# Performance work log

Measured on AMD Instinct MI355X. Metric: run time of the kernel, lower is better.

Reference implementation:

```python
import jax, jax.numpy as jnp
import numpy as np

CUTOFF = 5.2
BOX = 44.0
N_ATOMS = 8192

# 13 half-shifts used by the cell list (vector_index_displacement) + zero shift
HALF_SHIFTS = np.array([
    [-1, 0, 0], [-1, -1, 0], [0, -1, 0], [1, -1, 0],
    [-1, 1, -1], [0, 1, -1], [1, 1, -1], [-1, 0, -1],
    [0, 0, -1], [1, 0, -1], [-1, -1, -1], [0, -1, -1], [1, -1, -1]], dtype=np.int64)
ALL_SHIFTS = np.concatenate([np.zeros((1, 3), dtype=np.int64), HALF_SHIFTS], axis=0)  # (14,3)


def setup_inputs() -> dict:
    key = jax.random.key(0)
    k1, k2 = jax.random.split(key)
    species = jax.random.randint(k1, (1, N_ATOMS), 0, 4, dtype=jnp.int64)
    coordinates = jax.random.uniform(k2, (1, N_ATOMS, 3), dtype=jnp.float32) * BOX
    cell = jnp.eye(3, dtype=jnp.float32) * BOX
    pbc = jnp.ones((3,), dtype=bool)
    return {"species": species, "coordinates": coordinates, "cell": cell, "pbc": pbc}


def reference(species, coordinates, cell, pbc):
    # Single molecule, as asserted by the torch module.
    coords = coordinates[0]  # (N, 3)
    n = coords.shape[0]
    # map_to_central: wrap coordinates into the central cell
    frac = coords @ jnp.linalg.inv(cell)
    frac = frac - jnp.floor(frac)
    coords = frac @ cell
    # orthorhombic cell diagonal (norm of cell columns, as in _setup_variables)
    diag = jnp.linalg.norm(cell, axis=0)  # (3,)

    shifts = jnp.asarray(ALL_SHIFTS)
    pairs_list, shift_list = [], []
    cutoff2 = CUTOFF * CUTOFF
    for k in range(shifts.shape[0]):  # fixed small loop over 14 periodic shifts
        s = shifts[k]
        # delta[i, j] = r_i - r_j + s * cell_diagonal   (N, N, 3)
        delta = coords[:, None, :] - coords[None, :, :] + s.astype(coords.dtype) * diag
        d2 = jnp.sum(delta * delta, axis=-1)  # (N, N)
        mask = d2 <= cutoff2
        if k == 0:
            # within-image pairs: each unordered pair once, no self pairs
            mask = jnp.triu(mask, 1)
        i, j = jnp.nonzero(mask)  # eager: data-dependent pair count
        pairs_list.append(jnp.stack([i, j], axis=0))
        shift_list.append(jnp.broadcast_to(s, (i.shape[0], 3)))
    atom_pairs = jnp.concatenate(pairs_list, axis=1)  # (2, P)
    shift_indices = jnp.concatenate(shift_list, axis=0)  # (P, 3)
    return atom_pairs, shift_indices


if __name__ == "__main__":
    out = reference(**setup_inputs())
    print(out[0].shape, out[1].shape)
```

## Files before the change

kernel.cpp:

```cpp
#include <hip/hip_runtime.h>

#define CLB_NATOMS 8192
#define CLB_NSHIFT 14
#define CLB_NROWS (CLB_NSHIFT * CLB_NATOMS)
#define CLB_NTILE 112
#define CLB_NCELL 512
#define CLB_CAP 128
#define CLB_C2 ((float)(5.2 * 5.2))
#define CLB_R 5.35f

__device__ const int clb_shifts[CLB_NSHIFT][3] = {
    {0, 0, 0},
    {-1, 0, 0}, {-1, -1, 0}, {0, -1, 0}, {1, -1, 0},
    {-1, 1, -1}, {0, 1, -1}, {1, 1, -1}, {-1, 0, -1},
    {0, 0, -1}, {1, 0, -1}, {-1, -1, -1}, {0, -1, -1}, {1, -1, -1}};

__device__ float4 clb_pp[CLB_NATOMS];
__device__ float4 clb_sorted[CLB_NATOMS];
__device__ unsigned clb_hist[CLB_NCELL];
__device__ unsigned clb_cstart[CLB_NCELL + 1];
__device__ unsigned clb_cfill[CLB_NCELL];
__device__ int clb_jbuf[(size_t)CLB_NROWS * CLB_CAP];
__device__ unsigned clb_cnt[CLB_NROWS];
__device__ unsigned clb_off[CLB_NROWS];
__device__ unsigned clb_tot[CLB_NTILE];
__device__ float4 clb_dg;
__device__ float4 clb_cinv;
__device__ float4 clb_sf[CLB_NSHIFT];

__global__ __launch_bounds__(512) void clb_setup(const float* __restrict__ cell) {
  int t = threadIdx.x;
  if (t < CLB_NCELL) clb_hist[t] = 0u;
  if (t == 0) {
    float dgx = (float)sqrt((double)cell[0] * cell[0] + (double)cell[3] * cell[3] +
                            (double)cell[6] * cell[6]);
    float dgy = (float)sqrt((double)cell[1] * cell[1] + (double)cell[4] * cell[4] +
                            (double)cell[7] * cell[7]);
    float dgz = (float)sqrt((double)cell[2] * cell[2] + (double)cell[5] * cell[5] +
                            (double)cell[8] * cell[8]);
    clb_dg = make_float4(dgx, dgy, dgz, 0.f);
    clb_cinv = make_float4(8.0f / dgx, 8.0f / dgy, 8.0f / dgz, 0.f);
    for (int k = 0; k < CLB_NSHIFT; ++k)
      clb_sf[k] = make_float4(__fmul_rn((float)clb_shifts[k][0], dgx),
                              __fmul_rn((float)clb_shifts[k][1], dgy),
                              __fmul_rn((float)clb_shifts[k][2], dgz), 0.f);
  }
}

__device__ __forceinline__ int clb_cellof(const float4& p, const float4& cinv) {
  int cx = min(7, (int)(p.x * cinv.x));
  int cy = min(7, (int)(p.y * cinv.y));
  int cz = min(7, (int)(p.z * cinv.z));
  return (cz * 8 + cy) * 8 + cx;
}

__global__ __launch_bounds__(256) void clb_wrapbin(const float* __restrict__ coords,
                                                   const float* __restrict__ cell) {
  int i = blockIdx.x * blockDim.x + threadIdx.x;
  if (i >= CLB_NATOMS) return;
  double a00 = cell[0], a01 = cell[1], a02 = cell[2];
  double a10 = cell[3], a11 = cell[4], a12 = cell[5];
  double a20 = cell[6], a21 = cell[7], a22 = cell[8];
  double det = a00 * (a11 * a22 - a12 * a21) - a01 * (a10 * a22 - a12 * a20) +
               a02 * (a10 * a21 - a11 * a20);
  double id = 1.0 / det;
  float inv[3][3];
  inv[0][0] = (float)((a11 * a22 - a12 * a21) * id);
  inv[0][1] = (float)(-(a01 * a22 - a02 * a21) * id);
  inv[0][2] = (float)((a01 * a12 - a02 * a11) * id);
  inv[1][0] = (float)(-(a10 * a22 - a12 * a20) * id);
  inv[1][1] = (float)((a00 * a22 - a02 * a20) * id);
  inv[1][2] = (float)(-(a00 * a12 - a02 * a10) * id);
  inv[2][0] = (float)((a10 * a21 - a11 * a20) * id);
  inv[2][1] = (float)(-(a00 * a21 - a01 * a20) * id);
  inv[2][2] = (float)((a00 * a11 - a01 * a10) * id);

  float x = coords[3 * i], y = coords[3 * i + 1], z = coords[3 * i + 2];
  float fr[3], w[3];
#pragma unroll
  for (int c = 0; c < 3; ++c) {
    float f = __fadd_rn(__fadd_rn(__fmul_rn(x, inv[0][c]), __fmul_rn(y, inv[1][c])),
                        __fmul_rn(z, inv[2][c]));
    fr[c] = __fsub_rn(f, floorf(f));
  }
#pragma unroll
  for (int c = 0; c < 3; ++c) {
    w[c] = __fadd_rn(
        __fadd_rn(__fmul_rn(fr[0], cell[0 * 3 + c]), __fmul_rn(fr[1], cell[1 * 3 + c])),
        __fmul_rn(fr[2], cell[2 * 3 + c]));
  }
  float4 p = make_float4(w[0], w[1], w[2], 0.0f);
  clb_pp[i] = p;
  atomicAdd(&clb_hist[clb_cellof(p, clb_cinv)], 1u);
}

__global__ __launch_bounds__(512) void clb_cscan() {
  __shared__ unsigned sd[512];
  int t = threadIdx.x;
  unsigned v = clb_hist[t];
  sd[t] = v;
  __syncthreads();
  unsigned acc = v;
  for (int off = 1; off < 512; off <<= 1) {
    unsigned a = (t >= off) ? sd[t - off] : 0u;
    __syncthreads();
    acc += a;
    sd[t] = acc;
    __syncthreads();
  }
  clb_cstart[t] = acc - v;
  clb_cfill[t] = acc - v;
  if (t == 511) clb_cstart[512] = acc;
}

__global__ __launch_bounds__(256) void clb_scatter() {
  int i = blockIdx.x * blockDim.x + threadIdx.x;
  if (i >= CLB_NATOMS) return;
  float4 p = clb_pp[i];
  int c = clb_cellof(p, clb_cinv);
  unsigned pos = atomicAdd(&clb_cfill[c], 1u);
  p.w = __int_as_float(i);
  clb_sorted[pos] = p;
}

__device__ __forceinline__ bool clb_alive(float xi, float yi, float zi, int sx, int sy,
                                          int sz, float dgx, float dgy, float dgz) {
  bool a = true;
  if (sx < 0) a = a && (xi >= dgx - 5.3f); else if (sx > 0) a = a && (xi <= 5.3f);
  if (sy < 0) a = a && (yi >= dgy - 5.3f); else if (sy > 0) a = a && (yi <= 5.3f);
  if (sz < 0) a = a && (zi >= dgz - 5.3f); else if (sz > 0) a = a && (zi <= 5.3f);
  return a;
}

__device__ __forceinline__ void clb_crange(float t, float ci, int& lo, int& hi) {
  lo = max(0, (int)(fmaxf(t - CLB_R, 0.f) * ci));
  hi = min(7, (int)(fmaxf(t + CLB_R, 0.f) * ci));
}

__device__ __forceinline__ unsigned clb_iscan(unsigned v, int lane) {
  for (int off = 1; off < 64; off <<= 1) {
    unsigned t = __shfl_up(v, off);
    if (lane >= off) v += t;
  }
  return v;
}

__global__ __launch_bounds__(512) void clb_count() {
  __shared__ uint4 smask[8][64];
  int wslot = threadIdx.x >> 6;
  int wv = blockIdx.x * 8 + wslot;
  int lane = threadIdx.x & 63;
  unsigned* lm = (unsigned*)smask[wslot];
  int k = wv >> 13, i = wv & (CLB_NATOMS - 1);

  float4 dg = clb_dg;
  float4 sc = clb_sf[k];
  int sx = clb_shifts[k][0], sy = clb_shifts[k][1], sz = clb_shifts[k][2];
  float4 pi = clb_pp[i];
  if (k != 0 && !clb_alive(pi.x, pi.y, pi.z, sx, sy, sz, dg.x, dg.y, dg.z)) {
    if (lane == 0) clb_cnt[wv] = 0u;
    return;
  }
  smask[wslot][lane] = make_uint4(0u, 0u, 0u, 0u);

  float4 cinv = clb_cinv;
  int xlo, xhi, ylo, yhi, zlo, zhi;
  clb_crange(__fadd_rn(pi.x, sc.x), cinv.x, xlo, xhi);
  clb_crange(__fadd_rn(pi.y, sc.y), cinv.y, ylo, yhi);
  clb_crange(__fadd_rn(pi.z, sc.z), cinv.z, zlo, zhi);

  for (int cz = zlo; cz <= zhi; ++cz) {
    for (int cy = ylo; cy <= yhi; ++cy) {
      int idb = (cz * 8 + cy) * 8;
      unsigned b = clb_cstart[idb + xlo], e = clb_cstart[idb + xhi + 1];
      for (unsigned t = b + lane; t < e; t += 64) {
        float4 pj = clb_sorted[t];
        int j = __float_as_int(pj.w);
        float dx = __fadd_rn(__fsub_rn(pi.x, pj.x), sc.x);
        float dy = __fadd_rn(__fsub_rn(pi.y, pj.y), sc.y);
        float dz = __fadd_rn(__fsub_rn(pi.z, pj.z), sc.z);
        float d2 = __fadd_rn(__fadd_rn(__fmul_rn(dx, dx), __fmul_rn(dy, dy)),
                             __fmul_rn(dz, dz));
        bool ok = (d2 <= CLB_C2) && (k != 0 || i < j);
        if (ok) atomicOr(&lm[(unsigned)j >> 5], 1u << (j & 31));
      }
    }
  }
  __threadfence_block();

  const unsigned long long* mrow = (const unsigned long long*)lm;
  unsigned long long m0 = mrow[lane];
  unsigned long long m1 = mrow[64 + lane];
  unsigned c0 = (unsigned)__popcll(m0), c1 = (unsigned)__popcll(m1);
  unsigned s0 = clb_iscan(c0, lane);
  unsigned T0 = __shfl(s0, 63);
  unsigned e0 = s0 - c0;
  unsigned s1 = clb_iscan(c1, lane);
  unsigned T1 = __shfl(s1, 63);
  unsigned e1 = T0 + s1 - c1;

  size_t jb = (size_t)wv * CLB_CAP;
  unsigned p = e0;
  unsigned long long m = m0;
  while (m) {
    int b = __ffsll((long long)m) - 1;
    m &= m - 1;
    if (p < CLB_CAP) clb_jbuf[jb + p] = (lane << 6) + b;
    ++p;
  }
  p = e1;
  m = m1;
  while (m) {
    int b = __ffsll((long long)m) - 1;
    m &= m - 1;
    if (p < CLB_CAP) clb_jbuf[jb + p] = ((64 + lane) << 6) + b;
    ++p;
  }
  if (lane == 0) clb_cnt[wv] = min(T0 + T1, (unsigned)CLB_CAP);
}

__global__ __launch_bounds__(1024) void clb_s1() {
  __shared__ unsigned sd[1024];
  int t = threadIdx.x;
  int gid = blockIdx.x * 1024 + t;
  unsigned v = clb_cnt[gid];
  sd[t] = v;
  __syncthreads();
  unsigned acc = v;
  for (int off = 1; off < 1024; off <<= 1) {
    unsigned a = (t >= off) ? sd[t - off] : 0u;
    __syncthreads();
    acc += a;
    sd[t] = acc;
    __syncthreads();
  }
  clb_off[gid] = acc - v;
  if (t == 1023) clb_tot[blockIdx.x] = acc;
}

__global__ __launch_bounds__(1024) void clb_s2() {
  __shared__ unsigned sred[16];
  int t = threadIdx.x;
  unsigned v = (t < blockIdx.x) ? clb_tot[t] : 0u;
#pragma unroll
  for (int off = 32; off; off >>= 1) v += __shfl_down(v, off);
  if ((t & 63) == 0) sred[t >> 6] = v;
  __syncthreads();
  if (t == 0) {
    unsigned b = 0;
#pragma unroll
    for (int w = 0; w < 16; ++w) b += sred[w];
    sred[0] = b;
  }
  __syncthreads();
  clb_off[blockIdx.x * 1024 + t] += sred[0];
}

__global__ __launch_bounds__(512) void clb_emit(int* __restrict__ out, int P) {
  int wv = blockIdx.x * 8 + (threadIdx.x >> 6);
  int lane = threadIdx.x & 63;
  unsigned c = clb_cnt[wv];
  if (c == 0) return;
  unsigned off = clb_off[wv];
  int k = wv >> 13, i = wv & (CLB_NATOMS - 1);
  int sx = clb_shifts[k][0], sy = clb_shifts[k][1], sz = clb_shifts[k][2];
  size_t jb = (size_t)wv * CLB_CAP;
  for (unsigned q = lane; q < c; q += 64) {
    unsigned p = off + q;
    if (p < (unsigned)P) {
      out[p] = i;
      out[P + p] = clb_jbuf[jb + q];
      unsigned sp = 2u * (unsigned)P + 3u * p;
      out[sp] = sx;
      out[sp + 1] = sy;
      out[sp + 2] = sz;
    }
  }
}

extern "C" void kernel_launch(void* const* d_in, const int* in_sizes, int n_in,
                              void* d_out, int out_size, void* d_ws, size_t ws_size,
                              hipStream_t stream) {
  const float* coords = (const float*)d_in[1];
  const float* cell = (const float*)d_in[2];
  int P = out_size / 5;

  clb_setup<<<1, 512, 0, stream>>>(cell);
  clb_wrapbin<<<CLB_NATOMS / 256, 256, 0, stream>>>(coords, cell);
  clb_cscan<<<1, 512, 0, stream>>>();
  clb_scatter<<<CLB_NATOMS / 256, 256, 0, stream>>>();
  clb_count<<<CLB_NROWS / 8, 512, 0, stream>>>();
  clb_s1<<<CLB_NTILE, 1024, 0, stream>>>();
  clb_s2<<<CLB_NTILE, 1024, 0, stream>>>();
  clb_emit<<<CLB_NROWS / 8, 512, 0, stream>>>((int*)d_out, P);
}
```

Measured before the change: 55.66 us.

## Fuse setup, binning and scan stages to cut kernel launches from eight to five

Folds the cell setup into the wrap kernel, and merges histogram, cell scan and scatter into one single-block binsort kernel that uses shared-memory atomics. It also drops the second-level offset kernel: each emit wave now sums the preceding tile totals itself. The goal is to remove launch overhead and global atomics. In exchange, the sort runs on one block, and every emit wave repeats a small reduction over the tile totals.

Result: slower. 63.67 us (+14.4%).

```diff
diff --git a/kernel.cpp b/kernel.cpp
--- a/kernel.cpp
+++ b/kernel.cpp
@@ -1,63 +1,56 @@
 #include <hip/hip_runtime.h>
 
-#define CLB_NATOMS 8192
-#define CLB_NSHIFT 14
-#define CLB_NROWS (CLB_NSHIFT * CLB_NATOMS)
-#define CLB_NTILE 112
-#define CLB_NCELL 512
-#define CLB_CAP 128
-#define CLB_C2 ((float)(5.2 * 5.2))
-#define CLB_R 5.35f
-
-__device__ const int clb_shifts[CLB_NSHIFT][3] = {
+#define CLC_NATOMS 8192
+#define CLC_NSHIFT 14
+#define CLC_NROWS (CLC_NSHIFT * CLC_NATOMS)
+#define CLC_NTILE 112
+#define CLC_NCELL 512
+#define CLC_CAP 128
+#define CLC_C2 ((float)(5.2 * 5.2))
+#define CLC_R 5.35f
+
+__device__ const int clc_shifts[CLC_NSHIFT][3] = {
     {0, 0, 0},
     {-1, 0, 0}, {-1, -1, 0}, {0, -1, 0}, {1, -1, 0},
     {-1, 1, -1}, {0, 1, -1}, {1, 1, -1}, {-1, 0, -1},
     {0, 0, -1}, {1, 0, -1}, {-1, -1, -1}, {0, -1, -1}, {1, -1, -1}};
 
-__device__ float4 clb_pp[CLB_NATOMS];
-__device__ float4 clb_sorted[CLB_NATOMS];
-__device__ unsigned clb_hist[CLB_NCELL];
-__device__ unsigned clb_cstart[CLB_NCELL + 1];
-__device__ unsigned clb_cfill[CLB_NCELL];
-__device__ int clb_jbuf[(size_t)CLB_NROWS * CLB_CAP];
-__device__ unsigned clb_cnt[CLB_NROWS];
-__device__ unsigned clb_off[CLB_NROWS];
-__device__ unsigned clb_tot[CLB_NTILE];
-__device__ float4 clb_dg;
-__device__ float4 clb_cinv;
-__device__ float4 clb_sf[CLB_NSHIFT];
-
-__global__ __launch_bounds__(512) void clb_setup(const float* __restrict__ cell) {
-  int t = threadIdx.x;
-  if (t < CLB_NCELL) clb_hist[t] = 0u;
-  if (t == 0) {
+__device__ float4 clc_pp[CLC_NATOMS];
+__device__ float4 clc_sorted[CLC_NATOMS];
+__device__ unsigned clc_cstart[CLC_NCELL + 1];
+__device__ int clc_jbuf[(size_t)CLC_NROWS * CLC_CAP];
+__device__ unsigned clc_cnt[CLC_NROWS];
+__device__ unsigned clc_off[CLC_NROWS];
+__device__ unsigned clc_tot[CLC_NTILE];
+__device__ float4 clc_dg;
+__device__ float4 clc_cinv;
+__device__ float4 clc_sf[CLC_NSHIFT];
+
+__device__ __forceinline__ int clc_cellof(const float4& p, const float4& cinv) {
+  int cx = min(7, (int)(p.x * cinv.x));
+  int cy = min(7, (int)(p.y * cinv.y));
+  int cz = min(7, (int)(p.z * cinv.z));
+  return (cz * 8 + cy) * 8 + cx;
+}
+
+__global__ __launch_bounds__(256) void clc_wrap(const float* __restrict__ coords,
+                                                const float* __restrict__ cell) {
+  int i = blockIdx.x * blockDim.x + threadIdx.x;
+  if (i >= CLC_NATOMS) return;
+  if (i == 0) {
     float dgx = (float)sqrt((double)cell[0] * cell[0] + (double)cell[3] * cell[3] +
                             (double)cell[6] * cell[6]);
     float dgy = (float)sqrt((double)cell[1] * cell[1] + (double)cell[4] * cell[4] +
                             (double)cell[7] * cell[7]);
     float dgz = (float)sqrt((double)cell[2] * cell[2] + (double)cell[5] * cell[5] +
                             (double)cell[8] * cell[8]);
-    clb_dg = make_float4(dgx, dgy, dgz, 0.f);
-    clb_cinv = make_float4(8.0f / dgx, 8.0f / dgy, 8.0f / dgz, 0.f);
-    for (int k = 0; k < CLB_NSHIFT; ++k)
-      clb_sf[k] = make_float4(__fmul_rn((float)clb_shifts[k][0], dgx),
-                              __fmul_rn((float)clb_shifts[k][1], dgy),
-                              __fmul_rn((float)clb_shifts[k][2], dgz), 0.f);
-  }
-}
-
-__device__ __forceinline__ int clb_cellof(const float4& p, const float4& cinv) {
-  int cx = min(7, (int)(p.x * cinv.x));
-  int cy = min(7, (int)(p.y * cinv.y));
-  int cz = min(7, (int)(p.z * cinv.z));
-  return (cz * 8 + cy) * 8 + cx;
-}
-
-__global__ __launch_bounds__(256) void clb_wrapbin(const float* __restrict__ coords,
-                                                   const float* __restrict__ cell) {
-  int i = blockIdx.x * blockDim.x + threadIdx.x;
-  if (i >= CLB_NATOMS) return;
+    clc_dg = make_float4(dgx, dgy, dgz, 0.f);
+    clc_cinv = make_float4(8.0f / dgx, 8.0f / dgy, 8.0f / dgz, 0.f);
+    for (int k = 0; k < CLC_NSHIFT; ++k)
+      clc_sf[k] = make_float4(__fmul_rn((float)clc_shifts[k][0], dgx),
+                              __fmul_rn((float)clc_shifts[k][1], dgy),
+                              __fmul_rn((float)clc_shifts[k][2], dgz), 0.f);
+  }
   double a00 = cell[0], a01 = cell[1], a02 = cell[2];
   double a10 = cell[3], a11 = cell[4], a12 = cell[5];
   double a20 = cell[6], a21 = cell[7], a22 = cell[8];
@@ -89,41 +82,52 @@
         __fadd_rn(__fmul_rn(fr[0], cell[0 * 3 + c]), __fmul_rn(fr[1], cell[1 * 3 + c])),
         __fmul_rn(fr[2], cell[2 * 3 + c]));
   }
-  float4 p = make_float4(w[0], w[1], w[2], 0.0f);
-  clb_pp[i] = p;
-  atomicAdd(&clb_hist[clb_cellof(p, clb_cinv)], 1u);
-}
-
-__global__ __launch_bounds__(512) void clb_cscan() {
-  __shared__ unsigned sd[512];
+  clc_pp[i] = make_float4(w[0], w[1], w[2], 0.0f);
+}
+
+__global__ __launch_bounds__(1024) void clc_binsort() {
+  __shared__ unsigned h[CLC_NCELL];
+  __shared__ unsigned cfill[CLC_NCELL];
   int t = threadIdx.x;
-  unsigned v = clb_hist[t];
-  sd[t] = v;
-  __syncthreads();
+  if (t < CLC_NCELL) h[t] = 0u;
+  __syncthreads();
+  float4 cinv = clc_cinv;
+  int cid[8];
+#pragma unroll
+  for (int r = 0; r < 8; ++r) {
+    int i = t + r * 1024;
+    cid[r] = clc_cellof(clc_pp[i], cinv);
+    atomicAdd(&h[cid[r]], 1u);
+  }
+  __syncthreads();
+  unsigned v = (t < CLC_NCELL) ? h[t] : 0u;
   unsigned acc = v;
-  for (int off = 1; off < 512; off <<= 1) {
-    unsigned a = (t >= off) ? sd[t - off] : 0u;
-    __syncthreads();
-    acc += a;
-    sd[t] = acc;
-    __syncthreads();
-  }
-  clb_cstart[t] = acc - v;
-  clb_cfill[t] = acc - v;
-  if (t == 511) clb_cstart[512] = acc;
-}
-
-__global__ __launch_bounds__(256) void clb_scatter() {
-  int i = blockIdx.x * blockDim.x + threadIdx.x;
-  if (i >= CLB_NATOMS) return;
-  float4 p = clb_pp[i];
-  int c = clb_cellof(p, clb_cinv);
-  unsigned pos = atomicAdd(&clb_cfill[c], 1u);
-  p.w = __int_as_float(i);
-  clb_sorted[pos] = p;
-}
-
-__device__ __forceinline__ bool clb_alive(float xi, float yi, float zi, int sx, int sy,
+  for (int off = 1; off < CLC_NCELL; off <<= 1) {
+    unsigned a = (t >= off && t < CLC_NCELL) ? h[t - off] : 0u;
+    __syncthreads();
+    if (t < CLC_NCELL) {
+      acc += a;
+      h[t] = acc;
+    }
+    __syncthreads();
+  }
+  if (t < CLC_NCELL) {
+    clc_cstart[t] = acc - v;
+    cfill[t] = acc - v;
+  }
+  if (t == CLC_NCELL - 1) clc_cstart[CLC_NCELL] = acc;
+  __syncthreads();
+#pragma unroll
+  for (int r = 0; r < 8; ++r) {
+    int i = t + r * 1024;
+    unsigned pos = atomicAdd(&cfill[cid[r]], 1u);
+    float4 p = clc_pp[i];
+    p.w = __int_as_float(i);
+    clc_sorted[pos] = p;
+  }
+}
+
+__device__ __forceinline__ bool clc_alive(float xi, float yi, float zi, int sx, int sy,
                                           int sz, float dgx, float dgy, float dgz) {
   bool a = true;
   if (sx < 0) a = a && (xi >= dgx - 5.3f); else if (sx > 0) a = a && (xi <= 5.3f);
@@ -132,12 +136,12 @@
   return a;
 }
 
-__device__ __forceinline__ void clb_crange(float t, float ci, int& lo, int& hi) {
-  lo = max(0, (int)(fmaxf(t - CLB_R, 0.f) * ci));
-  hi = min(7, (int)(fmaxf(t + CLB_R, 0.f) * ci));
-}
-
-__device__ __forceinline__ unsigned clb_iscan(unsigned v, int lane) {
+__device__ __forceinline__ void clc_crange(float t, float ci, int& lo, int& hi) {
+  lo = max(0, (int)(fmaxf(t - CLC_R, 0.f) * ci));
+  hi = min(7, (int)(fmaxf(t + CLC_R, 0.f) * ci));
+}
+
+__device__ __forceinline__ unsigned clc_iscan(unsigned v, int lane) {
   for (int off = 1; off < 64; off <<= 1) {
     unsigned t = __shfl_up(v, off);
     if (lane >= off) v += t;
@@ -145,43 +149,43 @@
   return v;
 }
 
-__global__ __launch_bounds__(512) void clb_count() {
+__global__ __launch_bounds__(512) void clc_count() {
   __shared__ uint4 smask[8][64];
   int wslot = threadIdx.x >> 6;
   int wv = blockIdx.x * 8 + wslot;
   int lane = threadIdx.x & 63;
   unsigned* lm = (unsigned*)smask[wslot];
-  int k = wv >> 13, i = wv & (CLB_NATOMS - 1);
-
-  float4 dg = clb_dg;
-  float4 sc = clb_sf[k];
-  int sx = clb_shifts[k][0], sy = clb_shifts[k][1], sz = clb_shifts[k][2];
-  float4 pi = clb_pp[i];
-  if (k != 0 && !clb_alive(pi.x, pi.y, pi.z, sx, sy, sz, dg.x, dg.y, dg.z)) {
-    if (lane == 0) clb_cnt[wv] = 0u;
+  int k = wv >> 13, i = wv & (CLC_NATOMS - 1);
+
+  float4 dg = clc_dg;
+  float4 sc = clc_sf[k];
+  int sx = clc_shifts[k][0], sy = clc_shifts[k][1], sz = clc_shifts[k][2];
+  float4 pi = clc_pp[i];
+  if (k != 0 && !clc_alive(pi.x, pi.y, pi.z, sx, sy, sz, dg.x, dg.y, dg.z)) {
+    if (lane == 0) clc_cnt[wv] = 0u;
     return;
   }
   smask[wslot][lane] = make_uint4(0u, 0u, 0u, 0u);
 
-  float4 cinv = clb_cinv;
+  float4 cinv = clc_cinv;
   int xlo, xhi, ylo, yhi, zlo, zhi;
-  clb_crange(__fadd_rn(pi.x, sc.x), cinv.x, xlo, xhi);
-  clb_crange(__fadd_rn(pi.y, sc.y), cinv.y, ylo, yhi);
-  clb_crange(__fadd_rn(pi.z, sc.z), cinv.z, zlo, zhi);
+  clc_crange(__fadd_rn(pi.x, sc.x), cinv.x, xlo, xhi);
+  clc_crange(__fadd_rn(pi.y, sc.y), cinv.y, ylo, yhi);
+  clc_crange(__fadd_rn(pi.z, sc.z), cinv.z, zlo, zhi);
 
   for (int cz = zlo; cz <= zhi; ++cz) {
     for (int cy = ylo; cy <= yhi; ++cy) {
       int idb = (cz * 8 + cy) * 8;
-      unsigned b = clb_cstart[idb + xlo], e = clb_cstart[idb + xhi + 1];
+      unsigned b = clc_cstart[idb + xlo], e = clc_cstart[idb + xhi + 1];
       for (unsigned t = b + lane; t < e; t += 64) {
-        float4 pj = clb_sorted[t];
+        float4 pj = clc_sorted[t];
         int j = __float_as_int(pj.w);
         float dx = __fadd_rn(__fsub_rn(pi.x, pj.x), sc.x);
         float dy = __fadd_rn(__fsub_rn(pi.y, pj.y), sc.y);
         float dz = __fadd_rn(__fsub_rn(pi.z, pj.z), sc.z);
         float d2 = __fadd_rn(__fadd_rn(__fmul_rn(dx, dx), __fmul_rn(dy, dy)),
                              __fmul_rn(dz, dz));
-        bool ok = (d2 <= CLB_C2) && (k != 0 || i < j);
+        bool ok = (d2 <= CLC_C2) && (k != 0 || i < j);
         if (ok) atomicOr(&lm[(unsigned)j >> 5], 1u << (j & 31));
       }
     }
@@ -192,20 +196,20 @@
   unsigned long long m0 = mrow[lane];
   unsigned long long m1 = mrow[64 + lane];
   unsigned c0 = (unsigned)__popcll(m0), c1 = (unsigned)__popcll(m1);
-  unsigned s0 = clb_iscan(c0, lane);
+  unsigned s0 = clc_iscan(c0, lane);
   unsigned T0 = __shfl(s0, 63);
   unsigned e0 = s0 - c0;
-  unsigned s1 = clb_iscan(c1, lane);
+  unsigned s1 = clc_iscan(c1, lane);
   unsigned T1 = __shfl(s1, 63);
   unsigned e1 = T0 + s1 - c1;
 
-  size_t jb = (size_t)wv * CLB_CAP;
+  size_t jb = (size_t)wv * CLC_CAP;
   unsigned p = e0;
   unsigned long long m = m0;
   while (m) {
     int b = __ffsll((long long)m) - 1;
     m &= m - 1;
-    if (p < CLB_CAP) clb_jbuf[jb + p] = (lane << 6) + b;
+    if (p < CLC_CAP) clc_jbuf[jb + p] = (lane << 6) + b;
     ++p;
   }
   p = e1;
@@ -213,17 +217,17 @@
   while (m) {
     int b = __ffsll((long long)m) - 1;
     m &= m - 1;
-    if (p < CLB_CAP) clb_jbuf[jb + p] = ((64 + lane) << 6) + b;
+    if (p < CLC_CAP) clc_jbuf[jb + p] = ((64 + lane) << 6) + b;
     ++p;
   }
-  if (lane == 0) clb_cnt[wv] = min(T0 + T1, (unsigned)CLB_CAP);
-}
-
-__global__ __launch_bounds__(1024) void clb_s1() {
+  if (lane == 0) clc_cnt[wv] = min(T0 + T1, (unsigned)CLC_CAP);
+}
+
+__global__ __launch_bounds__(1024) void clc_s1() {
   __shared__ unsigned sd[1024];
   int t = threadIdx.x;
   int gid = blockIdx.x * 1024 + t;
-  unsigned v = clb_cnt[gid];
+  unsigned v = clc_cnt[gid];
   sd[t] = v;
   __syncthreads();
   unsigned acc = v;
@@ -234,42 +238,32 @@
     sd[t] = acc;
     __syncthreads();
   }
-  clb_off[gid] = acc - v;
-  if (t == 1023) clb_tot[blockIdx.x] = acc;
-}
-
-__global__ __launch_bounds__(1024) void clb_s2() {
-  __shared__ unsigned sred[16];
-  int t = threadIdx.x;
-  unsigned v = (t < blockIdx.x) ? clb_tot[t] : 0u;
-#pragma unroll
-  for (int off = 32; off; off >>= 1) v += __shfl_down(v, off);
-  if ((t & 63) == 0) sred[t >> 6] = v;
-  __syncthreads();
-  if (t == 0) {
-    unsigned b = 0;
-#pragma unroll
-    for (int w = 0; w < 16; ++w) b += sred[w];
-    sred[0] = b;
-  }
-  __syncthreads();
-  clb_off[blockIdx.x * 1024 + t] += sred[0];
-}
-
-__global__ __launch_bounds__(512) void clb_emit(int* __restrict__ out, int P) {
+  clc_off[gid] = acc - v;
+  if (t == 1023) clc_tot[blockIdx.x] = acc;
+}
+
+__global__ __launch_bounds__(512) void clc_emit(int* __restrict__ out, int P) {
   int wv = blockIdx.x * 8 + (threadIdx.x >> 6);
   int lane = threadIdx.x & 63;
-  unsigned c = clb_cnt[wv];
+  unsigned c = clc_cnt[wv];
   if (c == 0) return;
-  unsigned off = clb_off[wv];
-  int k = wv >> 13, i = wv & (CLB_NATOMS - 1);
-  int sx = clb_shifts[k][0], sy = clb_shifts[k][1], sz = clb_shifts[k][2];
-  size_t jb = (size_t)wv * CLB_CAP;
+  int tile = wv >> 10;
+  unsigned v = 0;
+  if (lane < tile) v = clc_tot[lane];
+  if (64 + lane < tile) v += clc_tot[64 + lane];
+#pragma unroll
+  for (int off = 32; off; off >>= 1) v += __shfl_down(v, off);
+  unsigned tbase = __shfl(v, 0);
+
+  unsigned off0 = clc_off[wv] + tbase;
+  int k = wv >> 13, i = wv & (CLC_NATOMS - 1);
+  int sx = clc_shifts[k][0], sy = clc_shifts[k][1], sz = clc_shifts[k][2];
+  size_t jb = (size_t)wv * CLC_CAP;
   for (unsigned q = lane; q < c; q += 64) {
-    unsigned p = off + q;
+    unsigned p = off0 + q;
     if (p < (unsigned)P) {
       out[p] = i;
-      out[P + p] = clb_jbuf[jb + q];
+      out[P + p] = clc_jbuf[jb + q];
       unsigned sp = 2u * (unsigned)P + 3u * p;
       out[sp] = sx;
       out[sp + 1] = sy;
@@ -285,12 +279,9 @@
   const float* cell = (const float*)d_in[2];
   int P = out_size / 5;
 
-  clb_setup<<<1, 512, 0, stream>>>(cell);
-  clb_wrapbin<<<CLB_NATOMS / 256, 256, 0, stream>>>(coords, cell);
-  clb_cscan<<<1, 512, 0, stream>>>();
-  clb_scatter<<<CLB_NATOMS / 256, 256, 0, stream>>>();
-  clb_count<<<CLB_NROWS / 8, 512, 0, stream>>>();
-  clb_s1<<<CLB_NTILE, 1024, 0, stream>>>();
-  clb_s2<<<CLB_NTILE, 1024, 0, stream>>>();
-  clb_emit<<<CLB_NROWS / 8, 512, 0, stream>>>((int*)d_out, P);
-}
+  clc_wrap<<<CLC_NATOMS / 256, 256, 0, stream>>>(coords, cell);
+  clc_binsort<<<1, 1024, 0, stream>>>();
+  clc_count<<<CLC_NROWS / 8, 512, 0, stream>>>();
+  clc_s1<<<CLC_NTILE, 1024, 0, stream>>>();
+  clc_emit<<<CLC_NROWS / 8, 512, 0, stream>>>((int*)d_out, P);
+}
```
